# Optimization experiments

Hardware: AMD Instinct MI355X
Metric: run time of the kernel (lower is better)

## Reference

```python
import jax, jax.numpy as jnp
import numpy as np
from jax import lax

WINDOW_SIZE = 11
SIGMA = 1.5
EPS = 1e-08
C1 = 0.01 ** 2
C2 = 0.03 ** 2


def _gaussian_window(ws, sigma):
    x = jnp.arange(ws, dtype=jnp.float32)
    g = jnp.exp(-((x - ws // 2) ** 2) / (2.0 * sigma ** 2))
    g = g / g.sum()
    w2d = jnp.outer(g, g)  # (ws, ws)
    return w2d[None, None]  # (1,1,ws,ws) OIHW depthwise kernel for C=1


def _normalize(a, b):
    # per-batch min-max normalize, matching torch code exactly
    B = a.shape[0]
    fa = a.reshape(B, -1)
    fb = b.reshape(B, -1)
    mn1 = fa.min(1).reshape(B, 1, 1, 1)
    mx1 = fa.max(1).reshape(B, 1, 1, 1)
    mn2 = fb.min(1).reshape(B, 1, 1, 1)
    mx2 = fb.max(1).reshape(B, 1, 1, 1)
    a = (a - mn1) / (mx1 - mn1 + EPS)
    b = (b - mn2) / (mx2 - mn2 + EPS)
    return a, b


def _dw_conv(x, win):
    # depthwise gaussian blur, SAME-style padding ws//2 (torch conv2d is xcorr;
    # gaussian kernel is symmetric so identical)
    C = x.shape[1]
    k = jnp.broadcast_to(win, (C, 1, WINDOW_SIZE, WINDOW_SIZE))
    pad = WINDOW_SIZE // 2
    return lax.conv_general_dilated(
        x, k, window_strides=(1, 1), padding=[(pad, pad), (pad, pad)],
        feature_group_count=C,
        dimension_numbers=('NCHW', 'OIHW', 'NCHW'))


def _ssim_mean(m1, m2, win):
    mu1 = _dw_conv(m1, win)
    mu2 = _dw_conv(m2, win)
    mu1_sq = mu1 * mu1
    mu2_sq = mu2 * mu2
    mu1_mu2 = mu1 * mu2
    sigma1 = _dw_conv(m1 * m1, win) - mu1_sq
    sigma2 = _dw_conv(m2 * m2, win) - mu2_sq
    sigma12 = _dw_conv(m1 * m2, win) - mu1_mu2
    ssim_map = ((2 * mu1_mu2 + C1) * (2 * sigma12 + C2)) / \
               ((mu1_sq + mu2_sq + C1) * (sigma1 + sigma2 + C2))
    return ssim_map.mean()


def _forward(img1, img2, mask_pos, w):
    B, C, H, W = img1.shape
    cols = mask_pos[:, None] + jnp.arange(w)  # (B, w)
    idx = cols[:, None, None, :]
    s1 = jnp.take_along_axis(img1, idx, axis=3)  # (B,C,H,w)
    s2 = jnp.take_along_axis(img2, idx, axis=3)

    # Faithful to source: normalize is called inside the per-batch loop, so
    # row b is normalized (B-b) times; zero rows stay zero (0/eps).
    def body(carry, b):
        m1, m2 = carry
        m1 = m1.at[b].set(s1[b])
        m2 = m2.at[b].set(s2[b])
        m1, m2 = _normalize(m1, m2)
        return (m1, m2), None

    init = (jnp.zeros_like(s1), jnp.zeros_like(s2))
    (m1, m2), _ = lax.scan(body, init, jnp.arange(B))
    win = _gaussian_window(WINDOW_SIZE, SIGMA)
    return _ssim_mean(m1, m2, win)


def setup_inputs() -> dict:
    key = jax.random.key(0)
    k1, k2, k3 = jax.random.split(key, 3)
    B, Cc, H, W = 8, 1, 1024, 2048
    w = 1024
    img1 = jax.random.uniform(k1, (B, Cc, H, W), dtype=jnp.float32)
    img2 = jax.random.uniform(k2, (B, Cc, H, W), dtype=jnp.float32)
    mask_pos = jax.random.randint(k3, (B,), 0, W - w, dtype=jnp.int64 if jax.config.jax_enable_x64 else jnp.int32)
    return {'img1': img1, 'img2': img2, 'mask_pos': mask_pos, 'mask_width': w}


def reference(img1, img2, mask_pos, mask_width):
    return _forward(img1, img2, mask_pos, int(mask_width))
```

## Files before the change

### kernel.cpp

```cpp
#include <hip/hip_runtime.h>

#define NB 8
#define IMH 1024
#define IMW 2048
#define WM 1024
#define RPB 32
#define CPB 256

__device__ __forceinline__ unsigned int enc_f(float f) {
    unsigned int u = __float_as_uint(f);
    return (u & 0x80000000u) ? ~u : (u | 0x80000000u);
}
__device__ __forceinline__ float dec_f(unsigned int u) {
    u = (u & 0x80000000u) ? (u & 0x7fffffffu) : ~u;
    return __uint_as_float(u);
}


__global__ void k_init(unsigned int* ws) {
    int t = threadIdx.x;
    if (t < 16) { ws[t] = 0xFFFFFFFFu; ws[16 + t] = 0u; }
    if (t == 0) *((double*)(ws + 80)) = 0.0;
}

__global__ __launch_bounds__(256) void k_minmax(const float* __restrict__ img1,
                                                const float* __restrict__ img2,
                                                const int* __restrict__ mask_pos,
                                                unsigned int* __restrict__ ws) {
    int bi = blockIdx.x >> 7;
    int img = bi >> 3, b = bi & 7;
    int rg = blockIdx.x & 127;
    const float* base = (img ? img2 : img1)
        + (size_t)b * (IMH * IMW) + (size_t)(rg * 8) * IMW + mask_pos[b];
    int tid = threadIdx.x;
    float mn = 3.4e38f, mx = -3.4e38f;
    for (int r = 0; r < 8; ++r) {
        const float* p = base + (size_t)r * IMW;
        unsigned mis = ((unsigned)(uintptr_t)p >> 2) & 3u;
        unsigned s = (4u - mis) & 3u;
        int nf4 = (int)((1024u - s) >> 2);
        if (tid < nf4) {
            float4 v = *(const float4*)(p + s + 4 * tid);
            mn = fminf(mn, fminf(fminf(v.x, v.y), fminf(v.z, v.w)));
            mx = fmaxf(mx, fmaxf(fmaxf(v.x, v.y), fmaxf(v.z, v.w)));
        }
        if (tid >= 248) {
            unsigned e = tid - 248;
            unsigned rem0 = s + 4u * (unsigned)nf4;
            unsigned tc = 1024u - rem0;
            unsigned idx = 0; bool ok = false;
            if (e < s) { idx = e; ok = true; }
            else if (e >= 4u && (e - 4u) < tc) { idx = rem0 + (e - 4u); ok = true; }
            if (ok) { float v = p[idx]; mn = fminf(mn, v); mx = fmaxf(mx, v); }
        }
    }
    for (int off = 32; off; off >>= 1) {
        mn = fminf(mn, __shfl_down(mn, off));
        mx = fmaxf(mx, __shfl_down(mx, off));
    }
    __shared__ float smn[4], smx[4];
    int lane = tid & 63, wid = tid >> 6;
    if (lane == 0) { smn[wid] = mn; smx[wid] = mx; }
    __syncthreads();
    if (tid == 0) {
        mn = fminf(fminf(smn[0], smn[1]), fminf(smn[2], smn[3]));
        mx = fmaxf(fmaxf(smx[0], smx[1]), fmaxf(smx[2], smx[3]));
        atomicMin(&ws[img * 8 + b], enc_f(mn));
        atomicMax(&ws[16 + img * 8 + b], enc_f(mx));
    }
}

__global__ __launch_bounds__(256) void k_ssim(const float* __restrict__ img1,
                                              const float* __restrict__ img2,
                                              const int* __restrict__ mask_pos,
                                              const unsigned int* __restrict__ ws,
                                              double* __restrict__ acc_g) {
    __shared__ float rb[2][1024];
    __shared__ float red[4];

    const int tid = threadIdx.x;
    const int b  = blockIdx.z;
    const int cb = blockIdx.x * CPB;
    const int r0 = blockIdx.y * RPB;
    const int mp = mask_pos[b];

    float mn1, sc1, mn2, sc2;
    {
        float mnA = dec_f(ws[b]),     mxA = dec_f(ws[16 + b]);
        float mnB = dec_f(ws[8 + b]), mxB = dec_f(ws[24 + b]);
        float rngA = mxA - mnA; float d0A = rngA + 1e-8f; double DA = (double)d0A; float MA = rngA / d0A;
        float rngB = mxB - mnB; float d0B = rngB + 1e-8f; double DB = (double)d0B; float MB = rngB / d0B;
        for (int j = 0; j < 7 - b; ++j) {
            float djA = MA + 1e-8f; DA *= (double)djA; MA = MA / djA;
            float djB = MB + 1e-8f; DB *= (double)djB; MB = MB / djB;
        }
        mn1 = mnA; sc1 = (float)(1.0 / DA);
        mn2 = mnB; sc2 = (float)(1.0 / DB);
    }
    float gw[11];
    {
        float s = 0.f;
#pragma unroll
        for (int k = 0; k < 11; ++k) {
            float x = (float)((k - 5) * (k - 5));
            gw[k] = expf(-x / 4.5f);
            s += gw[k];
        }
#pragma unroll
        for (int k = 0; k < 11; ++k) gw[k] = gw[k] / s;
    }

    const float* bs1 = img1 + (size_t)b * (IMH * IMW) + (ptrdiff_t)(r0 - 5) * IMW + mp;
    const float* bs2 = img2 + (size_t)b * (IMH * IMW) + (ptrdiff_t)(r0 - 5) * IMW + mp;

    const int mcA = cb + tid - 8;
    const bool okA = (unsigned)mcA < (unsigned)WM;
    const int mcB = cb + 248 + tid;
    const bool okB = (tid < 16) && ((unsigned)mcB < (unsigned)WM);
    unsigned voffA = (unsigned)(okA ? mcA : 0);
    unsigned voffB = (unsigned)(((unsigned)mcB < (unsigned)WM) ? mcB : 0);

    float acc[11][5];
#pragma unroll
    for (int s = 0; s < 11; ++s)
#pragma unroll
        for (int ch = 0; ch < 5; ++ch) acc[s][ch] = 0.f;
    float local = 0.f;

    const float* cur = &rb[0][0];
    float* nxt;

    {
        float va = 0.f, vb = 0.f, wa = 0.f, wb = 0.f;
        if ((unsigned)(r0 - 5) < (unsigned)IMH) {
            float x1 = bs1[voffA], x2 = bs2[voffA];
            float y1 = bs1[voffB], y2 = bs2[voffB];
            va = okA ? (x1 - mn1) * sc1 : 0.f;
            vb = okA ? (x2 - mn2) * sc2 : 0.f;
            wa = okB ? (y1 - mn1) * sc1 : 0.f;
            wb = okB ? (y2 - mn2) * sc2 : 0.f;
        }
        voffA += IMW; voffB += IMW;
        float* w0 = (float*)&rb[0][0];
        *(float2*)&w0[2 * tid] = make_float2(va, vb);
        *(float2*)&w0[2 * (256 + tid)] = make_float2(wa, wb);
        __syncthreads();
    }
    nxt = (float*)&rb[1][0];

#pragma unroll 1
    for (int g = 0; g < 4; ++g) {
#pragma unroll
        for (int p = 0; p < 11; ++p) {
            const int i = g * 11 + p;

            float va = 0.f, vb = 0.f, wa = 0.f, wb = 0.f;
            if ((unsigned)(r0 - 4 + i) < (unsigned)IMH) {
                float x1 = bs1[voffA], x2 = bs2[voffA];
                float y1 = bs1[voffB], y2 = bs2[voffB];
                va = okA ? (x1 - mn1) * sc1 : 0.f;
                vb = okA ? (x2 - mn2) * sc2 : 0.f;
                wa = okB ? (y1 - mn1) * sc1 : 0.f;
                wb = okB ? (y2 - mn2) * sc2 : 0.f;
            }
            voffA += IMW; voffB += IMW;

            float ha = 0.f, hbv = 0.f, haa = 0.f, hbb = 0.f, hab = 0.f;
#pragma unroll
            for (int k = 0; k < 11; ++k) {
                float2 e = *(const float2*)&cur[2 * (tid + 3 + k)];
                float av = e.x, bv = e.y, w = gw[k];
                ha  = fmaf(w, av, ha);
                hbv = fmaf(w, bv, hbv);
                haa = fmaf(w, av * av, haa);
                hbb = fmaf(w, bv * bv, hbb);
                hab = fmaf(w, av * bv, hab);
            }

#pragma unroll
            for (int s = 0; s < 11; ++s) {
                const float w = gw[(p + 10 - s) % 11];
                if (s == (p + 10) % 11) {
                    acc[s][0] = w * ha;  acc[s][1] = w * hbv; acc[s][2] = w * haa;
                    acc[s][3] = w * hbb; acc[s][4] = w * hab;
                } else {
                    acc[s][0] = fmaf(w, ha,  acc[s][0]);
                    acc[s][1] = fmaf(w, hbv, acc[s][1]);
                    acc[s][2] = fmaf(w, haa, acc[s][2]);
                    acc[s][3] = fmaf(w, hbb, acc[s][3]);
                    acc[s][4] = fmaf(w, hab, acc[s][4]);
                }
            }

            if (i >= 10 && i <= 41) {
                float mu1 = acc[p][0], mu2 = acc[p][1];
                float e11 = acc[p][2], e22 = acc[p][3], e12 = acc[p][4];
                float m11 = mu1 * mu1, m22 = mu2 * mu2, m12 = mu1 * mu2;
                float num = (2.f * m12 + 1e-4f) * (2.f * (e12 - m12) + 9e-4f);
                float den = (m11 + m22 + 1e-4f) * ((e11 - m11) + (e22 - m22) + 9e-4f);
                local += __fdividef(num, den);
            }

            *(float2*)&nxt[2 * tid] = make_float2(va, vb);
            *(float2*)&nxt[2 * (256 + tid)] = make_float2(wa, wb);
            __syncthreads();
            { const float* t = cur; cur = nxt; nxt = (float*)t; }
        }
    }

    for (int off = 32; off; off >>= 1) local += __shfl_down(local, off);
    int lane = tid & 63, wid = tid >> 6;
    if (lane == 0) red[wid] = local;
    __syncthreads();
    if (tid == 0) {
        double s = (double)red[0] + (double)red[1] + (double)red[2] + (double)red[3];
        atomicAdd(acc_g, s);
    }
}

__global__ void k_final(const double* __restrict__ acc, float* __restrict__ out) {
    out[0] = (float)(acc[0] * (1.0 / 8388608.0));
}

extern "C" void kernel_launch(void* const* d_in, const int* in_sizes, int n_in,
                              void* d_out, int out_size, void* d_ws, size_t ws_size,
                              hipStream_t stream) {
    const float* img1 = (const float*)d_in[0];
    const float* img2 = (const float*)d_in[1];
    const int* mask_pos = (const int*)d_in[2];
    unsigned int* ws = (unsigned int*)d_ws;
    double* acc = (double*)(ws + 80);
    float* out = (float*)d_out;

    hipLaunchKernelGGL(k_init, dim3(1), dim3(64), 0, stream, ws);
    hipLaunchKernelGGL(k_minmax, dim3(2048), dim3(256), 0, stream, img1, img2, mask_pos, ws);
    hipLaunchKernelGGL(k_ssim, dim3(WM / CPB, IMH / RPB, NB), dim3(256), 0, stream,
                       img1, img2, mask_pos, ws, acc);
    hipLaunchKernelGGL(k_final, dim3(1), dim3(1), 0, stream, acc, out);
}
```

Measured before the change: 218.2 us.

## Blur (a+b)^2 and (a-b)^2 instead of three products, prefetch rows two ahead

Reformulates the second-moment channels: the row buffer now stores a, b, (a+b)^2 and (a-b)^2, so only four blurred channels are needed instead of five, and sigma sums and cross terms are recovered algebraically. Global loads are issued one row further ahead (double-held register) so load latency overlaps more compute, and __syncthreads is replaced with an explicit lgkmcnt wait plus s_barrier. Halo loads are restricted to the 16 threads that need them, and trailing iterations that produce no output are skipped. The squared-sum form may lose some precision through cancellation, and the shared buffer grows to float4 per column.

```diff
diff --git a/kernel.cpp b/kernel.cpp
--- a/kernel.cpp
+++ b/kernel.cpp
@@ -6,6 +6,11 @@
 #define WM 1024
 #define RPB 32
 #define CPB 256
+
+#define ROW_BARRIER() do { \
+    asm volatile("s_waitcnt lgkmcnt(0)" ::: "memory"); \
+    __builtin_amdgcn_s_barrier(); \
+} while (0)
 
 __device__ __forceinline__ unsigned int enc_f(float f) {
     unsigned int u = __float_as_uint(f);
@@ -75,7 +80,7 @@
                                               const int* __restrict__ mask_pos,
                                               const unsigned int* __restrict__ ws,
                                               double* __restrict__ acc_g) {
-    __shared__ float rb[2][1024];
+    __shared__ float rb[2][272 * 4];
     __shared__ float red[4];
 
     const int tid = threadIdx.x;
@@ -116,95 +121,106 @@
     const int mcA = cb + tid - 8;
     const bool okA = (unsigned)mcA < (unsigned)WM;
     const int mcB = cb + 248 + tid;
-    const bool okB = (tid < 16) && ((unsigned)mcB < (unsigned)WM);
+    const bool okB = (unsigned)mcB < (unsigned)WM;
     unsigned voffA = (unsigned)(okA ? mcA : 0);
-    unsigned voffB = (unsigned)(((unsigned)mcB < (unsigned)WM) ? mcB : 0);
-
-    float acc[11][5];
-#pragma unroll
-    for (int s = 0; s < 11; ++s)
-#pragma unroll
-        for (int ch = 0; ch < 5; ++ch) acc[s][ch] = 0.f;
-    float local = 0.f;
-
-    const float* cur = &rb[0][0];
-    float* nxt;
-
-    {
+    unsigned voffB = (unsigned)(okB ? mcB : 0);
+
+    auto ldrow = [&](int rn, bool want, float4& out) {
         float va = 0.f, vb = 0.f, wa = 0.f, wb = 0.f;
-        if ((unsigned)(r0 - 5) < (unsigned)IMH) {
+        if (want && (unsigned)rn < (unsigned)IMH) {
             float x1 = bs1[voffA], x2 = bs2[voffA];
-            float y1 = bs1[voffB], y2 = bs2[voffB];
             va = okA ? (x1 - mn1) * sc1 : 0.f;
             vb = okA ? (x2 - mn2) * sc2 : 0.f;
-            wa = okB ? (y1 - mn1) * sc1 : 0.f;
-            wb = okB ? (y2 - mn2) * sc2 : 0.f;
+            if (tid < 16) {
+                float y1 = bs1[voffB], y2 = bs2[voffB];
+                wa = okB ? (y1 - mn1) * sc1 : 0.f;
+                wb = okB ? (y2 - mn2) * sc2 : 0.f;
+            }
         }
         voffA += IMW; voffB += IMW;
-        float* w0 = (float*)&rb[0][0];
-        *(float2*)&w0[2 * tid] = make_float2(va, vb);
-        *(float2*)&w0[2 * (256 + tid)] = make_float2(wa, wb);
-        __syncthreads();
-    }
-    nxt = (float*)&rb[1][0];
+        out = make_float4(va, vb, wa, wb);
+    };
+    auto commit = [&](float* buf, const float4& L) {
+        float pa = L.x + L.y, ma = L.x - L.y;
+        *(float4*)&buf[4 * tid] = make_float4(L.x, L.y, pa * pa, ma * ma);
+        if (tid < 16) {
+            float pb = L.z + L.w, mb = L.z - L.w;
+            *(float4*)&buf[4 * (256 + tid)] = make_float4(L.z, L.w, pb * pb, mb * mb);
+        }
+    };
+
+    float acc[11][4];
+#pragma unroll
+    for (int s = 0; s < 11; ++s)
+#pragma unroll
+        for (int ch = 0; ch < 4; ++ch) acc[s][ch] = 0.f;
+    float local = 0.f;
+
+    float4 held, fresh;
+    ldrow(r0 - 5, true, fresh);
+    ldrow(r0 - 4, true, held);
+    commit(&rb[0][0], fresh);
+    ROW_BARRIER();
+    const float* cur = &rb[0][0];
+    float* nxt = (float*)&rb[1][0];
+
+    const unsigned rdoff = 4u * (unsigned)(tid + 3);
 
 #pragma unroll 1
     for (int g = 0; g < 4; ++g) {
 #pragma unroll
         for (int p = 0; p < 11; ++p) {
+            if (g == 3 && p > 8) continue;
             const int i = g * 11 + p;
 
-            float va = 0.f, vb = 0.f, wa = 0.f, wb = 0.f;
-            if ((unsigned)(r0 - 4 + i) < (unsigned)IMH) {
-                float x1 = bs1[voffA], x2 = bs2[voffA];
-                float y1 = bs1[voffB], y2 = bs2[voffB];
-                va = okA ? (x1 - mn1) * sc1 : 0.f;
-                vb = okA ? (x2 - mn2) * sc2 : 0.f;
-                wa = okB ? (y1 - mn1) * sc1 : 0.f;
-                wb = okB ? (y2 - mn2) * sc2 : 0.f;
-            }
-            voffA += IMW; voffB += IMW;
-
-            float ha = 0.f, hbv = 0.f, haa = 0.f, hbb = 0.f, hab = 0.f;
-#pragma unroll
-            for (int k = 0; k < 11; ++k) {
-                float2 e = *(const float2*)&cur[2 * (tid + 3 + k)];
-                float av = e.x, bv = e.y, w = gw[k];
-                ha  = fmaf(w, av, ha);
-                hbv = fmaf(w, bv, hbv);
-                haa = fmaf(w, av * av, haa);
-                hbb = fmaf(w, bv * bv, hbb);
-                hab = fmaf(w, av * bv, hab);
+            float4 newL;
+            ldrow(r0 - 3 + i, (p <= 6) || (g < 3), newL);
+
+            float ha, hb2, hs, hd;
+            {
+                float4 e = *(const float4*)&cur[rdoff];
+                float w = gw[0];
+                ha = w * e.x; hb2 = w * e.y; hs = w * e.z; hd = w * e.w;
+#pragma unroll
+                for (int k = 1; k < 11; ++k) {
+                    float4 ek = *(const float4*)&cur[rdoff + 4u * k];
+                    float wk = gw[k];
+                    ha  = fmaf(wk, ek.x, ha);
+                    hb2 = fmaf(wk, ek.y, hb2);
+                    hs  = fmaf(wk, ek.z, hs);
+                    hd  = fmaf(wk, ek.w, hd);
+                }
             }
 
 #pragma unroll
             for (int s = 0; s < 11; ++s) {
                 const float w = gw[(p + 10 - s) % 11];
                 if (s == (p + 10) % 11) {
-                    acc[s][0] = w * ha;  acc[s][1] = w * hbv; acc[s][2] = w * haa;
-                    acc[s][3] = w * hbb; acc[s][4] = w * hab;
+                    acc[s][0] = w * ha;  acc[s][1] = w * hb2;
+                    acc[s][2] = w * hs;  acc[s][3] = w * hd;
                 } else {
                     acc[s][0] = fmaf(w, ha,  acc[s][0]);
-                    acc[s][1] = fmaf(w, hbv, acc[s][1]);
-                    acc[s][2] = fmaf(w, haa, acc[s][2]);
-                    acc[s][3] = fmaf(w, hbb, acc[s][3]);
-                    acc[s][4] = fmaf(w, hab, acc[s][4]);
+                    acc[s][1] = fmaf(w, hb2, acc[s][1]);
+                    acc[s][2] = fmaf(w, hs,  acc[s][2]);
+                    acc[s][3] = fmaf(w, hd,  acc[s][3]);
                 }
             }
 
-            if (i >= 10 && i <= 41) {
+            if ((g >= 1) || (p == 10)) {
                 float mu1 = acc[p][0], mu2 = acc[p][1];
-                float e11 = acc[p][2], e22 = acc[p][3], e12 = acc[p][4];
+                float sv  = acc[p][2], dv  = acc[p][3];
                 float m11 = mu1 * mu1, m22 = mu2 * mu2, m12 = mu1 * mu2;
-                float num = (2.f * m12 + 1e-4f) * (2.f * (e12 - m12) + 9e-4f);
-                float den = (m11 + m22 + 1e-4f) * ((e11 - m11) + (e22 - m22) + 9e-4f);
+                float sig12x2 = 0.5f * (sv - dv) - 2.f * m12;
+                float sigsum  = 0.5f * (sv + dv) - m11 - m22;
+                float num = (2.f * m12 + 1e-4f) * (sig12x2 + 9e-4f);
+                float den = (m11 + m22 + 1e-4f) * (sigsum + 9e-4f);
                 local += __fdividef(num, den);
             }
 
-            *(float2*)&nxt[2 * tid] = make_float2(va, vb);
-            *(float2*)&nxt[2 * (256 + tid)] = make_float2(wa, wb);
-            __syncthreads();
+            commit(nxt, held);
+            ROW_BARRIER();
             { const float* t = cur; cur = nxt; nxt = (float*)t; }
+            held = newL;
         }
     }
 
```

New measurement: 210.2 us. 3.7% less time.
